# Performance work log

Measured on AMD Instinct MI355X. Metric: run time of the kernel, lower is better.

Reference implementation:

```python
import jax, jax.numpy as jnp
import numpy as np

K = 1.0          # curvature of all manifolds
EPS = 1e-6
LN_EPS = 1e-5    # torch LayerNorm eps
POWER_K = 3.0

N_NODES, N_EDGES, IN_DIM, HID, HEADS = 50000, 250000, 128, 32, 4


def _time(s):
    # Lorentz time coordinate from space part
    return jnp.sqrt(jnp.sum(s * s, axis=-1, keepdims=True) + K)


def _hyp_point(s):
    return jnp.concatenate([_time(s), s], axis=-1)


def _layernorm(s, g, b):
    m = jnp.mean(s, axis=-1, keepdims=True)
    v = jnp.var(s, axis=-1, keepdims=True)
    return (s - m) / jnp.sqrt(v + LN_EPS) * g + b


def _fp(x, p=POWER_K):
    # ||x||_2 / ||x^p||_2 * x^p  (TransConv.fp)
    nx = jnp.sqrt(jnp.sum(x * x, axis=-1, keepdims=True))
    xp = x ** p
    nxp = jnp.sqrt(jnp.sum(xp * xp, axis=-1, keepdims=True))
    return nx / nxp * xp


def setup_inputs() -> dict:
    key = jax.random.key(0)
    ks = jax.random.split(key, 12)
    f32 = jnp.float32
    inp = {
        'h': jax.random.normal(ks[0], (N_NODES, IN_DIM), f32),
        'src': jax.random.randint(ks[1], (N_EDGES,), 0, N_NODES, jnp.int32),
        'dst': jax.random.randint(ks[2], (N_EDGES,), 0, N_NODES, jnp.int32),
        # fcs[0][0]: HypLinear(in_dim -> hidden), euclidean input (+1 time col)
        'W_fc': (jax.random.normal(ks[3], (IN_DIM + 1, HID), f32) / np.float32(np.sqrt(IN_DIM + 1))),
        'b_fc': jnp.zeros((HID,), f32),
        # bns[0]: HypLayerNorm(hidden)
        'ln1_g': jnp.ones((HID,), f32), 'ln1_b': jnp.zeros((HID,), f32),
        # Wq/Wk/Wv: per-head HypLinear(hidden -> hidden), input is (hidden+1)-dim point
        'Wq': jax.random.normal(ks[4], (HEADS, HID + 1, HID), f32) / np.float32(np.sqrt(HID + 1)),
        'bq': jnp.zeros((HEADS, HID), f32),
        'Wk': jax.random.normal(ks[5], (HEADS, HID + 1, HID), f32) / np.float32(np.sqrt(HID + 1)),
        'bk': jnp.zeros((HEADS, HID), f32),
        'Wv': jax.random.normal(ks[6], (HEADS, HID + 1, HID), f32) / np.float32(np.sqrt(HID + 1)),
        'bv': jnp.zeros((HEADS, HID), f32),
        # hidden_to_out[0]: HypLinear(hidden -> hidden)
        'W_ho': jax.random.normal(ks[7], (HID + 1, HID), f32) / np.float32(np.sqrt(HID + 1)),
        'b_ho': jnp.zeros((HID,), f32),
        # final HypLayerNorm (self.bn)
        'ln2_g': jnp.ones((HID,), f32), 'ln2_b': jnp.zeros((HID,), f32),
        'norm_scale': jnp.ones((), f32),
    }
    return inp


def reference(h, src, dst, W_fc, b_fc, ln1_g, ln1_b, Wq, bq, Wk, bk, Wv, bv,
              W_ho, b_ho, ln2_g, ln2_b, norm_scale):
    N = h.shape[0]
    # iter == 0: lift euclidean features, prepend ones for time column
    x1 = jnp.concatenate([jnp.ones_like(h[..., :1]), h], axis=-1)  # [N, IN+1]
    hyp = _hyp_point(x1 @ W_fc + b_fc)                             # [N, HID+1]
    residual = hyp
    # HypLayerNorm -> HypActivation(leaky_relu) -> HypDropout (eval: identity).
    # Intermediate time coords are recomputed/discarded; only the final point's
    # full (HID+1) coords feed the q/k/v HypLinears.
    s = jax.nn.leaky_relu(_layernorm(hyp[..., 1:], ln1_g, ln1_b))
    node = _hyp_point(s)                                           # [N, HID+1]
    # per-head HypLinear; edge_attention only uses the space part [:, :, 1:],
    # so the q/k/v time coords are never consumed and are omitted here.
    q = jnp.einsum('nt,htd->nhd', node, Wq) + bq                   # [N, H, HID]
    k = jnp.einsum('nt,htd->nhd', node, Wk) + bk
    v = jnp.einsum('nt,htd->nhd', node, Wv) + bv
    # gather to edges
    qe = q[dst]                                                    # [E, H, HID]
    ke = k[src]
    ve = v[src]
    inv_scale = 1.0 / jnp.abs(norm_scale)
    phi_q = _fp((jax.nn.leaky_relu(qe) + EPS) * inv_scale)
    phi_k = _fp((jax.nn.leaky_relu(ke) + EPS) * inv_scale)
    phi_v = (jax.nn.leaky_relu(ve) + EPS) * inv_scale
    # global (over all edges) kernelized linear attention moments
    ktv = jnp.einsum('ehm,ehd->hmd', phi_k, phi_v)                 # [H, HID, HID]
    numerator = jnp.einsum('ehm,hmd->ehd', phi_q, ktv)             # [E, H, HID]
    denominator = jnp.einsum('ehd,hd->eh', phi_q, jnp.sum(phi_k, axis=0))[..., None]
    attn = jnp.mean(numerator / (denominator + EPS), axis=1)       # [E, HID]
    t = jnp.sqrt(jnp.sum(attn * attn, axis=-1, keepdims=True) + K)
    edge_in = jnp.concatenate([t, attn], axis=-1)                  # [E, HID+1]
    edge_out = _hyp_point(edge_in @ W_ho + b_ho)                   # [E, HID+1]
    # fn.copy_e + fn.mean over incoming edges per destination node
    seg_sum = jax.ops.segment_sum(edge_out, dst, num_segments=N)
    cnt = jax.ops.segment_sum(jnp.ones((edge_out.shape[0], 1), edge_out.dtype), dst, num_segments=N)
    agg = jnp.where(cnt > 0, seg_sum / jnp.maximum(cnt, 1.0), 0.0)
    # Lorentz mid_point of (agg, residual)
    ave = 0.5 * (agg + residual)
    inner = -ave[..., :1] ** 2 + jnp.sum(ave[..., 1:] ** 2, axis=-1, keepdims=True)
    denom = jnp.sqrt(jnp.maximum(jnp.abs(inner), EPS))
    hnew = jnp.sqrt(K) * ave / denom
    # final HypLayerNorm + HypDropout(eval)
    out = _hyp_point(_layernorm(hnew[..., 1:], ln2_g, ln2_b))
    return out
```

## Files before the change

kernel.cpp:

```cpp
#include <hip/hip_runtime.h>

#define NN 50000
#define NE 250000
#define KTVC 4224
#define QKV_BLOCKS 256
#define PART_ROWS (QKV_BLOCKS * 2)

__device__ __forceinline__ float lrelu(float x) { return x > 0.f ? x : 0.01f * x; }

__global__ __launch_bounds__(256) void k_hist(const int* __restrict__ src,
                                              const int* __restrict__ dst,
                                              int* __restrict__ cnt_src,
                                              int* __restrict__ cnt_dst) {
    int e = blockIdx.x * 256 + threadIdx.x;
    if (e < NE) {
        atomicAdd(&cnt_src[src[e]], 1);
        atomicAdd(&cnt_dst[dst[e]], 1);
    }
}

__global__ __launch_bounds__(512) void k_fc(const float* __restrict__ h,
                                            const float* __restrict__ Wfc,
                                            const float* __restrict__ bfc,
                                            const float* __restrict__ g1,
                                            const float* __restrict__ b1,
                                            float* __restrict__ resid,
                                            float* __restrict__ node33T) {
    __shared__ float hch[128][33];
    __shared__ float stat_t[8][128];
    __shared__ float stat2_t[4][128];
    const int tid = threadIdx.x;
    const int q = __builtin_amdgcn_readfirstlane((threadIdx.x >> 7) & 3);
    const int nl = tid & 127;
    const int base = blockIdx.x * 128;
    const int n = base + nl;

    float acc[8];
#pragma unroll
    for (int jj = 0; jj < 8; ++jj) acc[jj] = Wfc[q * 8 + jj] + bfc[q * 8 + jj];

    for (int c = 0; c < 4; ++c) {
        __syncthreads();
#pragma unroll
        for (int r = 0; r < 8; ++r) {
            int idx = r * 512 + tid;
            int sn = idx >> 5, t = idx & 31;
            int gn = base + sn;
            hch[sn][t] = h[(size_t)((gn < NN) ? gn : 0) * 128 + c * 32 + t];
        }
        __syncthreads();
        for (int i = 0; i < 32; ++i) {
            float hv = hch[nl][i];
            const float* wr = Wfc + (size_t)(1 + c * 32 + i) * 32 + q * 8;
#pragma unroll
            for (int jj = 0; jj < 8; ++jj) acc[jj] = fmaf(hv, wr[jj], acc[jj]);
        }
    }
    float ps = 0.f, pq2 = 0.f;
#pragma unroll
    for (int jj = 0; jj < 8; ++jj) { ps += acc[jj]; pq2 += acc[jj] * acc[jj]; }
    stat_t[q * 2 + 0][nl] = ps;
    stat_t[q * 2 + 1][nl] = pq2;
    __syncthreads();
    float sm = stat_t[0][nl] + stat_t[2][nl] + stat_t[4][nl] + stat_t[6][nl];
    float sq = stat_t[1][nl] + stat_t[3][nl] + stat_t[5][nl] + stat_t[7][nl];
    float mean = sm * (1.f / 32.f);
    float var = fmaxf(sq * (1.f / 32.f) - mean * mean, 0.f);
    float rstd = rsqrtf(var + 1e-5f);
    float lr[8];
    float pl2 = 0.f;
#pragma unroll
    for (int jj = 0; jj < 8; ++jj) {
        int j = q * 8 + jj;
        float ln = (acc[jj] - mean) * rstd * g1[j] + b1[j];
        lr[jj] = lrelu(ln);
        pl2 += lr[jj] * lr[jj];
    }
    stat2_t[q][nl] = pl2;
    __syncthreads();
    float l2 = stat2_t[0][nl] + stat2_t[1][nl] + stat2_t[2][nl] + stat2_t[3][nl];
    if (n < NN) {
        float* rrow = resid + (size_t)n * 36;
#pragma unroll
        for (int jj = 0; jj < 8; ++jj) rrow[1 + q * 8 + jj] = acc[jj];
#pragma unroll
        for (int jj = 0; jj < 8; ++jj) node33T[(size_t)(1 + q * 8 + jj) * NN + n] = lr[jj];
        if (q == 0) {
            rrow[0] = sqrtf(sq + 1.f);
            node33T[n] = sqrtf(l2 + 1.f);
        }
    }
}

__global__ __launch_bounds__(512) void k_qkv(const float* __restrict__ node33T,
                                             const float* __restrict__ Wk, const float* __restrict__ bk,
                                             const float* __restrict__ Wv, const float* __restrict__ bv,
                                             const float* __restrict__ nscale,
                                             const int* __restrict__ cnt_src,
                                             float* __restrict__ partial) {
    __shared__ float nlds[64][37];
    __shared__ float pk[4][64][36];
    __shared__ float pv[4][64][36];
    const int tid = threadIdx.x;
    const int w_u = __builtin_amdgcn_readfirstlane(tid >> 6);
    const int m_u = w_u >> 2;
    const int h_u = w_u & 3;
    const int lane = tid & 63;
    const float inv = 1.f / fabsf(nscale[0]);
    const float* W = ((m_u == 0) ? Wk : Wv) + (size_t)h_u * 33 * 32;
    const float* bb = ((m_u == 0) ? bk : bv) + h_u * 32;
    const int mm4 = lane >> 3, d4 = lane & 7;

    float facc[16];
#pragma unroll
    for (int t = 0; t < 16; ++t) facc[t] = 0.f;
    float ks[4] = {0.f, 0.f, 0.f, 0.f};

    const int ntiles = (NN + 63) / 64;
    for (int tile = blockIdx.x; tile < ntiles; tile += QKV_BLOCKS) {
        const int base = tile * 64;
        const int n = base + lane;
#pragma unroll
        for (int r = 0; r < 5; ++r) {
            int idx = r * 512 + tid;
            if (idx < 2112) {
                int c = idx >> 6, sn = idx & 63;
                int gn = base + sn;
                nlds[sn][c] = node33T[(size_t)c * NN + ((gn < NN) ? gn : 0)];
            }
        }
        __syncthreads();

        float acc[32];
#pragma unroll
        for (int j = 0; j < 32; ++j) acc[j] = bb[j];
        for (int i = 0; i < 33; ++i) {
            float hv = nlds[lane][i];
            const float* wr = W + (size_t)i * 32;
#pragma unroll
            for (int j = 0; j < 32; ++j) acc[j] = fmaf(hv, wr[j], acc[j]);
        }

        if (m_u == 0) {
            const float wc = (n < NN) ? (float)cnt_src[n] : 0.f;
            float s2 = 0.f, s6 = 0.f;
#pragma unroll
            for (int j = 0; j < 32; ++j) {
                float x = (lrelu(acc[j]) + 1e-6f) * inv;
                s2 += x * x;
                float x3 = x * x * x;
                s6 += x3 * x3;
                acc[j] = x3;
            }
            const float factor = sqrtf(s2) / sqrtf(s6) * wc;
#pragma unroll
            for (int j = 0; j < 32; ++j) pk[h_u][lane][j] = factor * acc[j];
        } else {
#pragma unroll
            for (int j = 0; j < 32; ++j) pv[h_u][lane][j] = (lrelu(acc[j]) + 1e-6f) * inv;
        }
        __syncthreads();

#pragma unroll 4
        for (int n0 = 0; n0 < 32; ++n0) {
            const int nn = m_u * 32 + n0;
            float4 pkv = *(const float4*)&pk[h_u][nn][mm4 * 4];
            float4 pvv = *(const float4*)&pv[h_u][nn][d4 * 4];
            float pkv_a[4] = {pkv.x, pkv.y, pkv.z, pkv.w};
            float pvv_a[4] = {pvv.x, pvv.y, pvv.z, pvv.w};
#pragma unroll
            for (int i = 0; i < 4; ++i)
#pragma unroll
                for (int jj = 0; jj < 4; ++jj)
                    facc[i * 4 + jj] = fmaf(pkv_a[i], pvv_a[jj], facc[i * 4 + jj]);
            if (d4 == 0) {
#pragma unroll
                for (int i = 0; i < 4; ++i) ks[i] += pkv_a[i];
            }
        }
    }

    float* pb = partial + (size_t)(blockIdx.x * 2 + m_u) * KTVC;
#pragma unroll
    for (int i = 0; i < 4; ++i)
#pragma unroll
        for (int jj = 0; jj < 4; ++jj)
            pb[h_u * 1024 + (mm4 * 4 + i) * 32 + d4 * 4 + jj] = facc[i * 4 + jj];
    if (d4 == 0) {
#pragma unroll
        for (int i = 0; i < 4; ++i) pb[4096 + h_u * 32 + mm4 * 4 + i] = ks[i];
    }
}

__global__ __launch_bounds__(256) void k_red(const float* __restrict__ partial,
                                             float* __restrict__ ktvf) {
    __shared__ float red[8][33];
    const int tid = threadIdx.x;
    const int col = tid & 31, g = tid >> 5;
    const int c = blockIdx.x * 32 + col;
    float s = 0.f;
    for (int r = g * 64; r < (g + 1) * 64; ++r)
        s += partial[(size_t)r * KTVC + c];
    red[g][col] = s;
    __syncthreads();
    if (tid < 32) {
        float t0 = (red[0][tid] + red[1][tid]) + (red[2][tid] + red[3][tid]);
        float t1 = (red[4][tid] + red[5][tid]) + (red[6][tid] + red[7][tid]);
        ktvf[blockIdx.x * 32 + tid] = t0 + t1;
    }
}

__global__ __launch_bounds__(256) void k_final(const float* __restrict__ node33T,
                                               const float* __restrict__ Wq, const float* __restrict__ bq,
                                               const float* __restrict__ nscale,
                                               const float* __restrict__ ktvf,
                                               const float* __restrict__ Who,
                                               const float* __restrict__ bho,
                                               const float* __restrict__ g2,
                                               const float* __restrict__ b2,
                                               const int* __restrict__ cnt_dst,
                                               const float* __restrict__ resid,
                                               float* __restrict__ out) {
    __shared__ float nlds[64][37];
    __shared__ float att[4][64][33];
    __shared__ float who_lds[33 * 32];
    __shared__ float g2l[32], b2l[32], bhol[32];
    const int tid = threadIdx.x;
    const int h_u = __builtin_amdgcn_readfirstlane(tid >> 6);
    const int lane = tid & 63;
    const int base = blockIdx.x * 64;
    const float inv = 1.f / fabsf(nscale[0]);

#pragma unroll
    for (int r = 0; r < 9; ++r) {
        int idx = r * 256 + tid;
        if (idx < 2112) {
            int c = idx >> 6, sn = idx & 63;
            int gn = base + sn;
            nlds[sn][c] = node33T[(size_t)c * NN + ((gn < NN) ? gn : 0)];
        }
    }
    for (int f = tid; f < 33 * 32; f += 256) who_lds[f] = Who[f];
    if (tid < 32) { g2l[tid] = g2[tid]; b2l[tid] = b2[tid]; bhol[tid] = bho[tid]; }
    __syncthreads();

    {
        float acc[32];
#pragma unroll
        for (int j = 0; j < 32; ++j) acc[j] = bq[h_u * 32 + j];
        const float* W = Wq + (size_t)h_u * 33 * 32;
        for (int i = 0; i < 33; ++i) {
            float hv = nlds[lane][i];
            const float* wr = W + (size_t)i * 32;
#pragma unroll
            for (int j = 0; j < 32; ++j) acc[j] = fmaf(hv, wr[j], acc[j]);
        }
        float s2 = 0.f, s6 = 0.f;
#pragma unroll
        for (int j = 0; j < 32; ++j) {
            float x = (lrelu(acc[j]) + 1e-6f) * inv;
            s2 += x * x;
            float x3 = x * x * x;
            s6 += x3 * x3;
            acc[j] = x3;
        }
        const float factor = sqrtf(s2) / sqrtf(s6);
        const float* ksum = ktvf + 4096 + h_u * 32;
        float den = 0.f;
#pragma unroll
        for (int j = 0; j < 32; ++j) { acc[j] *= factor; den += acc[j] * ksum[j]; }
        const float rd = 0.25f / (den + 1e-6f);
        float num[32];
#pragma unroll
        for (int d = 0; d < 32; ++d) num[d] = 0.f;
        const float* kt = ktvf + h_u * 1024;
#pragma unroll 2
        for (int t = 0; t < 32; ++t) {
            const float f = acc[t];
            const float* kr = kt + t * 32;
#pragma unroll
            for (int d = 0; d < 32; ++d) num[d] = fmaf(f, kr[d], num[d]);
        }
#pragma unroll
        for (int d = 0; d < 32; ++d) att[h_u][lane][d] = num[d] * rd;
    }
    __syncthreads();

    const int nl2 = tid >> 2, jq = tid & 3;
    const int n2 = base + nl2;
    const int nc = (n2 < NN) ? n2 : NN - 1;
    float attn[32];
#pragma unroll
    for (int d = 0; d < 32; ++d)
        attn[d] = ((att[0][nl2][d] + att[1][nl2][d]) + (att[2][nl2][d] + att[3][nl2][d]));
    float a2 = 0.f;
#pragma unroll
    for (int d = 0; d < 32; ++d) a2 += attn[d] * attn[d];
    const float tc = sqrtf(a2 + 1.f);
    float eo[8];
#pragma unroll
    for (int jj = 0; jj < 8; ++jj) {
        int j = jq * 8 + jj;
        eo[jj] = bhol[j] + tc * who_lds[j];
    }
#pragma unroll
    for (int d = 0; d < 32; ++d) {
        const float f = attn[d];
        const float* wr = &who_lds[(1 + d) * 32 + jq * 8];
#pragma unroll
        for (int jj = 0; jj < 8; ++jj) eo[jj] = fmaf(f, wr[jj], eo[jj]);
    }
    float e2 = 0.f;
#pragma unroll
    for (int jj = 0; jj < 8; ++jj) e2 += eo[jj] * eo[jj];
    e2 += __shfl_xor(e2, 1);
    e2 += __shfl_xor(e2, 2);
    const float te = sqrtf(e2 + 1.f);
    const float sc = (cnt_dst[nc] > 0) ? 1.f : 0.f;
    const float* rr = resid + (size_t)nc * 36;
    const float av0 = 0.5f * (sc * te + rr[0]);
    float avs[8];
    float pinner = 0.f;
#pragma unroll
    for (int jj = 0; jj < 8; ++jj) {
        avs[jj] = 0.5f * (sc * eo[jj] + rr[1 + jq * 8 + jj]);
        pinner += avs[jj] * avs[jj];
    }
    pinner += __shfl_xor(pinner, 1);
    pinner += __shfl_xor(pinner, 2);
    const float inner = pinner - av0 * av0;
    const float rdn = 1.f / sqrtf(fmaxf(fabsf(inner), 1e-6f));
    float pm = 0.f;
#pragma unroll
    for (int jj = 0; jj < 8; ++jj) { avs[jj] *= rdn; pm += avs[jj]; }
    pm += __shfl_xor(pm, 1);
    pm += __shfl_xor(pm, 2);
    const float mean = pm * (1.f / 32.f);
    float pv2 = 0.f;
#pragma unroll
    for (int jj = 0; jj < 8; ++jj) { float dd = avs[jj] - mean; pv2 += dd * dd; }
    pv2 += __shfl_xor(pv2, 1);
    pv2 += __shfl_xor(pv2, 2);
    const float rstd = rsqrtf(pv2 * (1.f / 32.f) + 1e-5f);
    float ln[8];
    float pl2 = 0.f;
#pragma unroll
    for (int jj = 0; jj < 8; ++jj) {
        int j = jq * 8 + jj;
        ln[jj] = (avs[jj] - mean) * rstd * g2l[j] + b2l[j];
        pl2 += ln[jj] * ln[jj];
    }
    pl2 += __shfl_xor(pl2, 1);
    pl2 += __shfl_xor(pl2, 2);
    if (n2 < NN) {
        float* orow = out + (size_t)n2 * 33;
#pragma unroll
        for (int jj = 0; jj < 8; ++jj) orow[1 + jq * 8 + jj] = ln[jj];
        if (jq == 0) orow[0] = sqrtf(pl2 + 1.f);
    }
}

extern "C" void kernel_launch(void* const* d_in, const int* in_sizes, int n_in,
                              void* d_out, int out_size, void* d_ws, size_t ws_size,
                              hipStream_t stream) {
    const float* h   = (const float*)d_in[0];
    const int* src   = (const int*)d_in[1];
    const int* dst   = (const int*)d_in[2];
    const float* Wfc = (const float*)d_in[3];
    const float* bfc = (const float*)d_in[4];
    const float* g1  = (const float*)d_in[5];
    const float* b1  = (const float*)d_in[6];
    const float* Wq  = (const float*)d_in[7];
    const float* bq  = (const float*)d_in[8];
    const float* Wk  = (const float*)d_in[9];
    const float* bk  = (const float*)d_in[10];
    const float* Wv  = (const float*)d_in[11];
    const float* bv  = (const float*)d_in[12];
    const float* Who = (const float*)d_in[13];
    const float* bho = (const float*)d_in[14];
    const float* g2  = (const float*)d_in[15];
    const float* b2  = (const float*)d_in[16];
    const float* nsc = (const float*)d_in[17];
    float* out = (float*)d_out;
    char* ws = (char*)d_ws;

    int* cnt_src   = (int*)(ws + 0);
    int* cnt_dst   = (int*)(ws + 200000);
    float* resid   = (float*)(ws + 400000);
    float* node33T = (float*)(ws + 7600000);
    float* part    = (float*)(ws + 14200000);
    float* ktvf    = (float*)(ws + 22852608);

    hipMemsetAsync(ws, 0, 400000, stream);
    hipLaunchKernelGGL(k_hist, dim3((NE + 255) / 256), dim3(256), 0, stream,
                       src, dst, cnt_src, cnt_dst);
    hipLaunchKernelGGL(k_fc, dim3((NN + 127) / 128), dim3(512), 0, stream,
                       h, Wfc, bfc, g1, b1, resid, node33T);
    hipLaunchKernelGGL(k_qkv, dim3(QKV_BLOCKS), dim3(512), 0, stream,
                       node33T, Wk, bk, Wv, bv, nsc, cnt_src, part);
    hipLaunchKernelGGL(k_red, dim3(KTVC / 32), dim3(256), 0, stream,
                       part, ktvf);
    hipLaunchKernelGGL(k_final, dim3((NN + 63) / 64), dim3(256), 0, stream,
                       node33T, Wq, bq, nsc, ktvf, Who, bho, g2, b2, cnt_dst, resid, out);
}
```

Before: 144.1 us.

## Split k_qkv across heads via a 2D grid with small blocks and in-block partial merging

```diff
diff --git a/kernel.cpp b/kernel.cpp
--- a/kernel.cpp
+++ b/kernel.cpp
@@ -3,8 +3,7 @@
 #define NN 50000
 #define NE 250000
 #define KTVC 4224
-#define QKV_BLOCKS 256
-#define PART_ROWS (QKV_BLOCKS * 2)
+#define NBX 512
 
 __device__ __forceinline__ float lrelu(float x) { return x > 0.f ? x : 0.01f * x; }
 
@@ -92,23 +91,22 @@
     }
 }
 
-__global__ __launch_bounds__(512) void k_qkv(const float* __restrict__ node33T,
+__global__ __launch_bounds__(128) void k_qkv(const float* __restrict__ node33T,
                                              const float* __restrict__ Wk, const float* __restrict__ bk,
                                              const float* __restrict__ Wv, const float* __restrict__ bv,
                                              const float* __restrict__ nscale,
                                              const int* __restrict__ cnt_src,
                                              float* __restrict__ partial) {
-    __shared__ float nlds[64][37];
-    __shared__ float pk[4][64][36];
-    __shared__ float pv[4][64][36];
+    __shared__ float nlds[64][33];
+    __shared__ float pk[64][36];
+    __shared__ float pv[64][36];
     const int tid = threadIdx.x;
     const int w_u = __builtin_amdgcn_readfirstlane(tid >> 6);
-    const int m_u = w_u >> 2;
-    const int h_u = w_u & 3;
+    const int h_u = __builtin_amdgcn_readfirstlane(blockIdx.y);
     const int lane = tid & 63;
     const float inv = 1.f / fabsf(nscale[0]);
-    const float* W = ((m_u == 0) ? Wk : Wv) + (size_t)h_u * 33 * 32;
-    const float* bb = ((m_u == 0) ? bk : bv) + h_u * 32;
+    const float* W = ((w_u == 0) ? Wk : Wv) + (size_t)h_u * 33 * 32;
+    const float* bb = ((w_u == 0) ? bk : bv) + h_u * 32;
     const int mm4 = lane >> 3, d4 = lane & 7;
 
     float facc[16];
@@ -117,17 +115,13 @@
     float ks[4] = {0.f, 0.f, 0.f, 0.f};
 
     const int ntiles = (NN + 63) / 64;
-    for (int tile = blockIdx.x; tile < ntiles; tile += QKV_BLOCKS) {
+    for (int tile = blockIdx.x; tile < ntiles; tile += NBX) {
         const int base = tile * 64;
         const int n = base + lane;
-#pragma unroll
-        for (int r = 0; r < 5; ++r) {
-            int idx = r * 512 + tid;
-            if (idx < 2112) {
-                int c = idx >> 6, sn = idx & 63;
-                int gn = base + sn;
-                nlds[sn][c] = node33T[(size_t)c * NN + ((gn < NN) ? gn : 0)];
-            }
+        for (int idx = tid; idx < 2112; idx += 128) {
+            int c = idx >> 6, sn = idx & 63;
+            int gn = base + sn;
+            nlds[sn][c] = node33T[(size_t)c * NN + ((gn < NN) ? gn : 0)];
         }
         __syncthreads();
 
@@ -141,7 +135,7 @@
             for (int j = 0; j < 32; ++j) acc[j] = fmaf(hv, wr[j], acc[j]);
         }
 
-        if (m_u == 0) {
+        if (w_u == 0) {
             const float wc = (n < NN) ? (float)cnt_src[n] : 0.f;
             float s2 = 0.f, s6 = 0.f;
 #pragma unroll
@@ -154,18 +148,18 @@
             }
             const float factor = sqrtf(s2) / sqrtf(s6) * wc;
 #pragma unroll
-            for (int j = 0; j < 32; ++j) pk[h_u][lane][j] = factor * acc[j];
+            for (int j = 0; j < 32; ++j) pk[lane][j] = factor * acc[j];
         } else {
 #pragma unroll
-            for (int j = 0; j < 32; ++j) pv[h_u][lane][j] = (lrelu(acc[j]) + 1e-6f) * inv;
+            for (int j = 0; j < 32; ++j) pv[lane][j] = (lrelu(acc[j]) + 1e-6f) * inv;
         }
         __syncthreads();
 
 #pragma unroll 4
         for (int n0 = 0; n0 < 32; ++n0) {
-            const int nn = m_u * 32 + n0;
-            float4 pkv = *(const float4*)&pk[h_u][nn][mm4 * 4];
-            float4 pvv = *(const float4*)&pv[h_u][nn][d4 * 4];
+            const int nn = w_u * 32 + n0;
+            float4 pkv = *(const float4*)&pk[nn][mm4 * 4];
+            float4 pvv = *(const float4*)&pv[nn][d4 * 4];
             float pkv_a[4] = {pkv.x, pkv.y, pkv.z, pkv.w};
             float pvv_a[4] = {pvv.x, pvv.y, pvv.z, pvv.w};
 #pragma unroll
@@ -178,17 +172,33 @@
                 for (int i = 0; i < 4; ++i) ks[i] += pkv_a[i];
             }
         }
-    }
-
-    float* pb = partial + (size_t)(blockIdx.x * 2 + m_u) * KTVC;
-#pragma unroll
-    for (int i = 0; i < 4; ++i)
-#pragma unroll
-        for (int jj = 0; jj < 4; ++jj)
-            pb[h_u * 1024 + (mm4 * 4 + i) * 32 + d4 * 4 + jj] = facc[i * 4 + jj];
-    if (d4 == 0) {
-#pragma unroll
-        for (int i = 0; i < 4; ++i) pb[4096 + h_u * 32 + mm4 * 4 + i] = ks[i];
+        __syncthreads();
+    }
+
+    float* scr = &pk[0][0];
+    float* scr2 = &pv[0][0];
+    if (w_u == 0) {
+#pragma unroll
+        for (int t = 0; t < 16; ++t) scr[lane * 16 + t] = facc[t];
+        if (d4 == 0) {
+#pragma unroll
+            for (int i = 0; i < 4; ++i) scr2[mm4 * 4 + i] = ks[i];
+        }
+    }
+    __syncthreads();
+    if (w_u == 1) {
+        float* pb = partial + (size_t)blockIdx.x * KTVC + h_u * 1056;
+#pragma unroll
+        for (int i = 0; i < 4; ++i)
+#pragma unroll
+            for (int jj = 0; jj < 4; ++jj)
+                pb[(mm4 * 4 + i) * 32 + d4 * 4 + jj] =
+                    facc[i * 4 + jj] + scr[lane * 16 + i * 4 + jj];
+        if (d4 == 0) {
+#pragma unroll
+            for (int i = 0; i < 4; ++i)
+                pb[1024 + mm4 * 4 + i] = ks[i] + scr2[mm4 * 4 + i];
+        }
     }
 }
 
@@ -265,7 +275,7 @@
             acc[j] = x3;
         }
         const float factor = sqrtf(s2) / sqrtf(s6);
-        const float* ksum = ktvf + 4096 + h_u * 32;
+        const float* ksum = ktvf + h_u * 1056 + 1024;
         float den = 0.f;
 #pragma unroll
         for (int j = 0; j < 32; ++j) { acc[j] *= factor; den += acc[j] * ksum[j]; }
@@ -273,7 +283,7 @@
         float num[32];
 #pragma unroll
         for (int d = 0; d < 32; ++d) num[d] = 0.f;
-        const float* kt = ktvf + h_u * 1024;
+        const float* kt = ktvf + h_u * 1056;
 #pragma unroll 2
         for (int t = 0; t < 32; ++t) {
             const float f = acc[t];
@@ -396,7 +406,7 @@
                        src, dst, cnt_src, cnt_dst);
     hipLaunchKernelGGL(k_fc, dim3((NN + 127) / 128), dim3(512), 0, stream,
                        h, Wfc, bfc, g1, b1, resid, node33T);
-    hipLaunchKernelGGL(k_qkv, dim3(QKV_BLOCKS), dim3(512), 0, stream,
+    hipLaunchKernelGGL(k_qkv, dim3(NBX, 4), dim3(128), 0, stream,
                        node33T, Wk, bk, Wv, bv, nsc, cnt_src, part);
     hipLaunchKernelGGL(k_red, dim3(KTVC / 32), dim3(256), 0, stream,
                        part, ktvf);
```

Result: faster. 126.9 us (-12.0%).
